# Kernel tuning notes

Hardware: AMD Instinct MI355X
Metric: run time of the kernel (lower is better)

The kernel has to match this reference:

```python
import jax, jax.numpy as jnp
import numpy as np

B, N, D = 16, 4096, 128          # graphs, points per graph, feature dim
RATIO = 0.25
M = int(N * RATIO)               # 1024 sampled points per graph (static)
RADIUS = 0.2


def setup_inputs() -> dict:
    key = jax.random.key(0)
    k1, k2 = jax.random.split(key)
    x = jax.random.normal(k1, (B * N, D), dtype=jnp.float32)
    pos = jax.random.uniform(k2, (B * N, 3), dtype=jnp.float32)  # unit cube
    batch = jnp.repeat(jnp.arange(B, dtype=jnp.int32), N)        # sorted, equal-size graphs
    return {"x": x, "pos": pos, "batch": batch}


def _fps(pos_g):
    """Farthest point sampling on one graph. pos_g: [N,3] -> [M] int indices.
    Deterministic start at index 0 (random_start=False, i.e. eval mode)."""
    def step(carry, _):
        dist, last = carry
        d = jnp.sum((pos_g - pos_g[last]) ** 2, axis=-1)   # [N]
        dist = jnp.minimum(dist, d)                        # dist to nearest selected
        nxt = jnp.argmax(dist).astype(jnp.int32)
        return (dist, nxt), last
    init = (jnp.full((pos_g.shape[0],), jnp.inf, pos_g.dtype), jnp.int32(0))
    _, idx = jax.lax.scan(step, init, None, length=M)
    return idx  # [M]


def reference(x, pos, batch):
    # Equal-size graphs -> reshape instead of segment bookkeeping.
    pos_b = pos.reshape(B, N, 3)
    x_b = x.reshape(B, N, D)

    # FPS per graph, vmapped (sequential greedy selection inside lax.scan).
    idx = jax.vmap(_fps)(pos_b)                                    # [B, M]

    sampled_pos = jnp.take_along_axis(pos_b, idx[:, :, None], axis=1)  # [B, M, 3]
    sampled_x = jnp.take_along_axis(x_b, idx[:, :, None], axis=1)      # [B, M, D]

    # radius_graph within each graph: boolean adjacency (j within r of i, no self loops).
    diff = sampled_pos[:, :, None, :] - sampled_pos[:, None, :, :]     # [B, M, M, 3]
    d2 = jnp.sum(diff * diff, axis=-1)                                 # [B, M, M]
    adj = (d2 <= RADIUS * RADIUS) & ~jnp.eye(M, dtype=bool)[None]      # [B, M, M]

    sampled_batch = jnp.repeat(jnp.arange(B, dtype=batch.dtype), M)    # [B*M]
    return (sampled_x.reshape(B * M, D),
            sampled_pos.reshape(B * M, 3),
            sampled_batch,
            adj)
```

## Files before the change

kernel.cpp:

```cpp
#include <hip/hip_runtime.h>
#include <stdint.h>

#define BB 16
#define NN 4096
#define DD 128
#define MM 1024
#define RADIUS2 0.04f
#define TPB 512
#define PPT 8
#define NW  (TPB / 64)

typedef unsigned long long u64;
typedef unsigned int u32;
typedef unsigned int uint2v __attribute__((ext_vector_type(2)));

__device__ __forceinline__ u64 umax64(u64 a, u64 b) { return a > b ? a : b; }

template <int CTRL>
__device__ __forceinline__ u64 dpp_max(u64 v) {
    u32 lo = (u32)__builtin_amdgcn_update_dpp(0, (int)(u32)v,         CTRL, 0xF, 0xF, true);
    u32 hi = (u32)__builtin_amdgcn_update_dpp(0, (int)(u32)(v >> 32), CTRL, 0xF, 0xF, true);
    return umax64(v, ((u64)hi << 32) | lo);
}

__device__ __forceinline__ u64 swz16_max(u64 v) {
    u32 lo = (u32)__builtin_amdgcn_ds_swizzle((int)(u32)v,         0x401F);
    u32 hi = (u32)__builtin_amdgcn_ds_swizzle((int)(u32)(v >> 32), 0x401F);
    return umax64(v, ((u64)hi << 32) | lo);
}

__device__ __forceinline__ u64 swap32_max(u64 v) {
#if __has_builtin(__builtin_amdgcn_permlane32_swap)
    uint2v lo = __builtin_amdgcn_permlane32_swap((u32)v,         (u32)v,         false, false);
    uint2v hi = __builtin_amdgcn_permlane32_swap((u32)(v >> 32), (u32)(v >> 32), false, false);
    u64 a = ((u64)hi[0] << 32) | (u64)lo[0];
    u64 b = ((u64)hi[1] << 32) | (u64)lo[1];
    return umax64(a, b);
#else
    return umax64(v, __shfl_xor(v, 32, 64));
#endif
}

__device__ __forceinline__ u64 wave_max(u64 k) {
    k = dpp_max<0xB1>(k);
    k = dpp_max<0x4E>(k);
    k = dpp_max<0x141>(k);
    k = dpp_max<0x140>(k);
    k = swz16_max(k);
    k = swap32_max(k);
    return k;
}

__global__ __launch_bounds__(TPB) void fps_kernel(const float* __restrict__ pos,
                                                  int* __restrict__ idx_out) {
    const int b    = blockIdx.x;
    const int tid  = threadIdx.x;
    const int wid  = tid >> 6;
    const int lane = tid & 63;

    __shared__ float4 pos4[NN];
    __shared__ u64 partials[2][NW];

    const float* pg = pos + (size_t)b * NN * 3;
    for (int k = tid; k < NN * 3; k += TPB)
        ((float*)&pos4[k / 3])[k % 3] = pg[k];
    __syncthreads();

    float px[PPT], py[PPT], pz[PPT], dist[PPT];
#pragma unroll
    for (int j = 0; j < PPT; ++j) {
        float4 p = pos4[tid * PPT + j];
        px[j] = p.x; py[j] = p.y; pz[j] = p.z;
        dist[j] = __builtin_inff();
    }

    const u32 idx_base = 0xFFFFFFFFu - (u32)(tid * PPT);
    int last = 0;

    for (int m = 0; m < MM; ++m) {
        if (tid == 0) idx_out[b * MM + m] = last;
        if (m == MM - 1) break;

        float4 lp = pos4[last];
        float lx = lp.x, ly = lp.y, lz = lp.z;

        u64 k[PPT];
#pragma unroll
        for (int j = 0; j < PPT; ++j) {
            float dx = px[j] - lx;
            float dy = py[j] - ly;
            float dz = pz[j] - lz;
            float d = __fadd_rn(__fadd_rn(__fmul_rn(dx, dx), __fmul_rn(dy, dy)),
                                __fmul_rn(dz, dz));
            dist[j] = fminf(dist[j], d);
            k[j] = ((u64)__float_as_uint(dist[j]) << 32) | (u64)(idx_base - (u32)j);
        }
#pragma unroll
        for (int s = PPT / 2; s > 0; s >>= 1)
#pragma unroll
            for (int j = 0; j < s; ++j) k[j] = umax64(k[j], k[j + s]);

        u64 key = wave_max(k[0]);

        const int buf = m & 1;
        if (lane == 0) partials[buf][wid] = key;
        __syncthreads();

        u64 t0[NW];
#pragma unroll
        for (int w = 0; w < NW; ++w) t0[w] = partials[buf][w];
#pragma unroll
        for (int s = NW / 2; s > 0; s >>= 1)
#pragma unroll
            for (int w = 0; w < s; ++w) t0[w] = umax64(t0[w], t0[w + s]);

        last = (int)(0xFFFFFFFFu - (u32)(t0[0] & 0xFFFFFFFFull));
    }
}

__global__ void gather_x_kernel(const float* __restrict__ x,
                                const int* __restrict__ idx,
                                float* __restrict__ out) {
    int t = blockIdx.x * blockDim.x + threadIdx.x;
    if (t >= BB * MM * DD / 4) return;
    int row = t >> 5;
    int c4  = (t & 31) << 2;
    int b   = row >> 10;
    int n   = idx[row];
    const float4 v = *(const float4*)(x + ((size_t)(b * NN + n) * DD + c4));
    *(float4*)(out + (size_t)row * DD + c4) = v;
}

__global__ void gather_pb_kernel(const float* __restrict__ pos,
                                 const int* __restrict__ idx,
                                 float* __restrict__ spos,
                                 float* __restrict__ sbatch) {
    int r = blockIdx.x * blockDim.x + threadIdx.x;
    if (r >= BB * MM) return;
    int b = r >> 10;
    int n = idx[r];
    const float* p = pos + (size_t)(b * NN + n) * 3;
    spos[r * 3 + 0] = p[0];
    spos[r * 3 + 1] = p[1];
    spos[r * 3 + 2] = p[2];
    sbatch[r] = (float)b;
}

__global__ void adj_kernel(const float* __restrict__ spos,
                           float* __restrict__ adj) {
    int row = blockIdx.x;
    int b   = row >> 10;
    int i   = row & (MM - 1);
    const float* pb = spos + (size_t)b * MM * 3;
    float xi = pb[i * 3 + 0];
    float yi = pb[i * 3 + 1];
    float zi = pb[i * 3 + 2];

    int j0 = threadIdx.x << 2;
    float4 r;
    float* o = adj + (size_t)row * MM;
#pragma unroll
    for (int k = 0; k < 4; ++k) {
        int j = j0 + k;
        float dx = xi - pb[j * 3 + 0];
        float dy = yi - pb[j * 3 + 1];
        float dz = zi - pb[j * 3 + 2];
        float d2 = __fadd_rn(__fadd_rn(__fmul_rn(dx, dx), __fmul_rn(dy, dy)),
                             __fmul_rn(dz, dz));
        float v = (d2 <= RADIUS2 && j != i) ? 1.0f : 0.0f;
        ((float*)&r)[k] = v;
    }
    *(float4*)(o + j0) = r;
}

extern "C" void kernel_launch(void* const* d_in, const int* in_sizes, int n_in,
                              void* d_out, int out_size, void* d_ws, size_t ws_size,
                              hipStream_t stream) {
    const float* x   = (const float*)d_in[0];
    const float* pos = (const float*)d_in[1];

    float* out    = (float*)d_out;
    int*   idx_ws = (int*)d_ws;

    float* sx   = out;
    float* spos = sx + (size_t)BB * MM * DD;
    float* sbat = spos + (size_t)BB * MM * 3;
    float* adj  = sbat + (size_t)BB * MM;

    fps_kernel<<<BB, TPB, 0, stream>>>(pos, idx_ws);
    gather_x_kernel<<<(BB * MM * DD / 4 + 255) / 256, 256, 0, stream>>>(x, idx_ws, sx);
    gather_pb_kernel<<<(BB * MM + 255) / 256, 256, 0, stream>>>(pos, idx_ws, spos, sbat);
    adj_kernel<<<BB * MM, 256, 0, stream>>>(spos, adj);
}
```

Measured before the change: 822.6 us.

## Split FPS argmax into float max then index min, use packed f32x2 distance math

The FPS block shrinks to 256 threads with 16 points per thread, and distance updates use two-wide float vectors so the compiler can emit packed FP32 ops. The 64-bit key argmax, which needed paired 32-bit DPP and swizzle steps, becomes a 32-bit float wave max followed by a 32-bit min over candidate indices. The final cross-wave combine picks the first wave whose max equals the global max. Fewer threads mean fewer waves per barrier but more serial work per thread and more register pressure, and the two reductions add a second dependent shuffle chain.

Measured after the change: 690.0 us. -16.1%, faster.

```diff
diff --git a/kernel.cpp b/kernel.cpp
--- a/kernel.cpp
+++ b/kernel.cpp
@@ -6,49 +6,56 @@
 #define DD 128
 #define MM 1024
 #define RADIUS2 0.04f
-#define TPB 512
-#define PPT 8
+#define TPB 256
+#define PPT 16
+#define NPAIR (PPT / 2)
 #define NW  (TPB / 64)
 
 typedef unsigned long long u64;
 typedef unsigned int u32;
+typedef float f32x2 __attribute__((ext_vector_type(2)));
 typedef unsigned int uint2v __attribute__((ext_vector_type(2)));
 
-__device__ __forceinline__ u64 umax64(u64 a, u64 b) { return a > b ? a : b; }
+__device__ __forceinline__ u32 umin2(u32 a, u32 b) { return a < b ? a : b; }
+__device__ __forceinline__ u32 umin3(u32 a, u32 b, u32 c) { return umin2(umin2(a, b), c); }
+__device__ __forceinline__ float fmax3(float a, float b, float c) { return fmaxf(fmaxf(a, b), c); }
 
 template <int CTRL>
-__device__ __forceinline__ u64 dpp_max(u64 v) {
-    u32 lo = (u32)__builtin_amdgcn_update_dpp(0, (int)(u32)v,         CTRL, 0xF, 0xF, true);
-    u32 hi = (u32)__builtin_amdgcn_update_dpp(0, (int)(u32)(v >> 32), CTRL, 0xF, 0xF, true);
-    return umax64(v, ((u64)hi << 32) | lo);
-}
-
-__device__ __forceinline__ u64 swz16_max(u64 v) {
-    u32 lo = (u32)__builtin_amdgcn_ds_swizzle((int)(u32)v,         0x401F);
-    u32 hi = (u32)__builtin_amdgcn_ds_swizzle((int)(u32)(v >> 32), 0x401F);
-    return umax64(v, ((u64)hi << 32) | lo);
-}
-
-__device__ __forceinline__ u64 swap32_max(u64 v) {
+__device__ __forceinline__ float dpp_fmax(float v) {
+    int o = __builtin_amdgcn_update_dpp(0, __float_as_int(v), CTRL, 0xF, 0xF, true);
+    return fmaxf(v, __int_as_float(o));
+}
+__device__ __forceinline__ float wave_fmax(float v) {
+    v = dpp_fmax<0xB1>(v);
+    v = dpp_fmax<0x4E>(v);
+    v = dpp_fmax<0x141>(v);
+    v = dpp_fmax<0x140>(v);
+    { int o = __builtin_amdgcn_ds_swizzle(__float_as_int(v), 0x401F); v = fmaxf(v, __int_as_float(o)); }
 #if __has_builtin(__builtin_amdgcn_permlane32_swap)
-    uint2v lo = __builtin_amdgcn_permlane32_swap((u32)v,         (u32)v,         false, false);
-    uint2v hi = __builtin_amdgcn_permlane32_swap((u32)(v >> 32), (u32)(v >> 32), false, false);
-    u64 a = ((u64)hi[0] << 32) | (u64)lo[0];
-    u64 b = ((u64)hi[1] << 32) | (u64)lo[1];
-    return umax64(a, b);
+    { uint2v r = __builtin_amdgcn_permlane32_swap(__float_as_uint(v), __float_as_uint(v), false, false);
+      v = fmaxf(__uint_as_float(r[0]), __uint_as_float(r[1])); }
 #else
-    return umax64(v, __shfl_xor(v, 32, 64));
+    v = fmaxf(v, __shfl_xor(v, 32, 64));
 #endif
-}
-
-__device__ __forceinline__ u64 wave_max(u64 k) {
-    k = dpp_max<0xB1>(k);
-    k = dpp_max<0x4E>(k);
-    k = dpp_max<0x141>(k);
-    k = dpp_max<0x140>(k);
-    k = swz16_max(k);
-    k = swap32_max(k);
-    return k;
+    return v;
+}
+template <int CTRL>
+__device__ __forceinline__ u32 dpp_umin(u32 v) {
+    u32 o = (u32)__builtin_amdgcn_update_dpp(0, (int)v, CTRL, 0xF, 0xF, true);
+    return umin2(v, o);
+}
+__device__ __forceinline__ u32 wave_umin(u32 v) {
+    v = dpp_umin<0xB1>(v);
+    v = dpp_umin<0x4E>(v);
+    v = dpp_umin<0x141>(v);
+    v = dpp_umin<0x140>(v);
+    { u32 o = (u32)__builtin_amdgcn_ds_swizzle((int)v, 0x401F); v = umin2(v, o); }
+#if __has_builtin(__builtin_amdgcn_permlane32_swap)
+    { uint2v r = __builtin_amdgcn_permlane32_swap(v, v, false, false); v = umin2(r[0], r[1]); }
+#else
+    v = umin2(v, __shfl_xor(v, 32, 64));
+#endif
+    return v;
 }
 
 __global__ __launch_bounds__(TPB) void fps_kernel(const float* __restrict__ pos,
@@ -66,15 +73,23 @@
         ((float*)&pos4[k / 3])[k % 3] = pg[k];
     __syncthreads();
 
-    float px[PPT], py[PPT], pz[PPT], dist[PPT];
-#pragma unroll
-    for (int j = 0; j < PPT; ++j) {
-        float4 p = pos4[tid * PPT + j];
-        px[j] = p.x; py[j] = p.y; pz[j] = p.z;
-        dist[j] = __builtin_inff();
-    }
-
-    const u32 idx_base = 0xFFFFFFFFu - (u32)(tid * PPT);
+    f32x2 px[NPAIR], py[NPAIR], pz[NPAIR];
+    float dist[PPT];
+    u32 idxs[PPT];
+#pragma unroll
+    for (int j = 0; j < NPAIR; ++j) {
+        float4 a = pos4[tid * PPT + 2 * j];
+        float4 c = pos4[tid * PPT + 2 * j + 1];
+        px[j] = (f32x2){a.x, c.x};
+        py[j] = (f32x2){a.y, c.y};
+        pz[j] = (f32x2){a.z, c.z};
+    }
+#pragma unroll
+    for (int k = 0; k < PPT; ++k) {
+        dist[k] = __builtin_inff();
+        idxs[k] = (u32)(tid * PPT + k);
+    }
+
     int last = 0;
 
     for (int m = 0; m < MM; ++m) {
@@ -82,39 +97,63 @@
         if (m == MM - 1) break;
 
         float4 lp = pos4[last];
-        float lx = lp.x, ly = lp.y, lz = lp.z;
-
-        u64 k[PPT];
-#pragma unroll
-        for (int j = 0; j < PPT; ++j) {
-            float dx = px[j] - lx;
-            float dy = py[j] - ly;
-            float dz = pz[j] - lz;
-            float d = __fadd_rn(__fadd_rn(__fmul_rn(dx, dx), __fmul_rn(dy, dy)),
-                                __fmul_rn(dz, dz));
-            dist[j] = fminf(dist[j], d);
-            k[j] = ((u64)__float_as_uint(dist[j]) << 32) | (u64)(idx_base - (u32)j);
+        f32x2 lx = {lp.x, lp.x}, ly = {lp.y, lp.y}, lz = {lp.z, lp.z};
+
+        {
+#pragma clang fp contract(off)
+#pragma unroll
+            for (int j = 0; j < NPAIR; ++j) {
+                f32x2 dx = px[j] - lx;
+                f32x2 dy = py[j] - ly;
+                f32x2 dz = pz[j] - lz;
+                f32x2 d  = dx * dx + dy * dy;
+                d = d + dz * dz;
+                dist[2 * j]     = fminf(dist[2 * j],     d.x);
+                dist[2 * j + 1] = fminf(dist[2 * j + 1], d.y);
+            }
         }
-#pragma unroll
-        for (int s = PPT / 2; s > 0; s >>= 1)
-#pragma unroll
-            for (int j = 0; j < s; ++j) k[j] = umax64(k[j], k[j + s]);
-
-        u64 key = wave_max(k[0]);
+
+        float t0 = fmax3(dist[0],  dist[1],  dist[2]);
+        float t1 = fmax3(dist[3],  dist[4],  dist[5]);
+        float t2 = fmax3(dist[6],  dist[7],  dist[8]);
+        float t3 = fmax3(dist[9],  dist[10], dist[11]);
+        float t4 = fmax3(dist[12], dist[13], dist[14]);
+        float tmax = fmax3(fmax3(t0, t1, t2), fmaxf(t3, t4), dist[15]);
+
+        float wmax = wave_fmax(tmax);
+
+        u32 c[PPT];
+#pragma unroll
+        for (int k = 0; k < PPT; ++k)
+            c[k] = (dist[k] == wmax) ? idxs[k] : 0xFFFFFFFFu;
+        u32 s0 = umin3(c[0],  c[1],  c[2]);
+        u32 s1 = umin3(c[3],  c[4],  c[5]);
+        u32 s2 = umin3(c[6],  c[7],  c[8]);
+        u32 s3 = umin3(c[9],  c[10], c[11]);
+        u32 s4 = umin3(c[12], c[13], c[14]);
+        u32 cand = umin3(umin3(s0, s1, s2), umin2(s3, s4), c[15]);
+
+        u32 widx = wave_umin(cand);
 
         const int buf = m & 1;
-        if (lane == 0) partials[buf][wid] = key;
+        if (lane == 0)
+            partials[buf][wid] = ((u64)__float_as_uint(wmax) << 32) | (u64)widx;
         __syncthreads();
 
-        u64 t0[NW];
-#pragma unroll
-        for (int w = 0; w < NW; ++w) t0[w] = partials[buf][w];
-#pragma unroll
-        for (int s = NW / 2; s > 0; s >>= 1)
-#pragma unroll
-            for (int w = 0; w < s; ++w) t0[w] = umax64(t0[w], t0[w + s]);
-
-        last = (int)(0xFFFFFFFFu - (u32)(t0[0] & 0xFFFFFFFFull));
+        u64 e0 = partials[buf][0];
+        u64 e1 = partials[buf][1];
+        u64 e2 = partials[buf][2];
+        u64 e3 = partials[buf][3];
+        float m0 = __uint_as_float((u32)(e0 >> 32));
+        float m1 = __uint_as_float((u32)(e1 >> 32));
+        float m2 = __uint_as_float((u32)(e2 >> 32));
+        float m3 = __uint_as_float((u32)(e3 >> 32));
+        float g  = fmaxf(fmaxf(m0, m1), fmaxf(m2, m3));
+        u32 li = (u32)e3;
+        li = (m2 == g) ? (u32)e2 : li;
+        li = (m1 == g) ? (u32)e1 : li;
+        li = (m0 == g) ? (u32)e0 : li;
+        last = (int)li;
     }
 }
 
```
